# Optimization experiments

Hardware: AMD Instinct MI355X
Metric: run time of the kernel (lower is better)

The kernel has to match this reference:

```python
import jax, jax.numpy as jnp
import numpy as np

D_MODEL = 1024
NUM_HEADS = 16
HEAD_DIM = D_MODEL // NUM_HEADS
WINDOW = 256
NEG = -1000000000.0


def setup_inputs() -> dict:
    key = jax.random.key(0)
    ks = jax.random.split(key, 9)
    B, N, D = 2, 2048, D_MODEL
    s = 1.0 / np.sqrt(D)
    inp = {
        "x": jax.random.normal(ks[0], (B, N, D), dtype=jnp.float32),
        "Wq": jax.random.normal(ks[1], (D, D), dtype=jnp.float32) * s,
        "bq": jnp.zeros((D,), dtype=jnp.float32),
        "Wk": jax.random.normal(ks[2], (D, D), dtype=jnp.float32) * s,
        "bk": jnp.zeros((D,), dtype=jnp.float32),
        "Wv": jax.random.normal(ks[3], (D, D), dtype=jnp.float32) * s,
        "bv": jnp.zeros((D,), dtype=jnp.float32),
        "Wo": jax.random.normal(ks[4], (D, D), dtype=jnp.float32) * s,
        "bo": jnp.zeros((D,), dtype=jnp.float32),
    }
    return inp


def reference(x, Wq, bq, Wk, bk, Wv, bv, Wo, bo):
    B, N, D = x.shape
    H, hd = NUM_HEADS, HEAD_DIM
    q = (x @ Wq + bq).reshape(B, N, H, hd).transpose(0, 2, 1, 3)  # [B,H,N,hd]
    k = (x @ Wk + bk).reshape(B, N, H, hd).transpose(0, 2, 1, 3)
    v = (x @ Wv + bv).reshape(B, N, H, hd).transpose(0, 2, 1, 3)

    i = jnp.arange(N)[:, None]
    j = jnp.arange(N)[None, :]
    blocked = (j > i) | (j < i - WINDOW)  # causal + local window
    mask = jnp.where(blocked, jnp.float32(NEG), jnp.float32(0.0))  # [N,N]

    logits = jnp.einsum("bhid,bhjd->bhij", q, k) / jnp.sqrt(jnp.float32(hd))
    logits = logits + mask[None, None, :, :]
    attn = jax.nn.softmax(logits, axis=-1)
    out = jnp.einsum("bhij,bhjd->bhid", attn, v)  # [B,H,N,hd]
    out = out.transpose(0, 2, 1, 3).reshape(B, N, D)
    return out @ Wo + bo
```

## Files before the change

kernel.cpp:

```cpp
#include <hip/hip_runtime.h>


typedef unsigned short ushort_t;
typedef __bf16 bf16x8 __attribute__((ext_vector_type(8)));
typedef float f32x4 __attribute__((ext_vector_type(4)));
typedef unsigned short ushort8 __attribute__((ext_vector_type(8)));
typedef unsigned short ushort4v __attribute__((ext_vector_type(4)));

#define LOG2E 1.4426950408889634f

static __device__ __forceinline__ ushort_t f2b(float f) {
    union { float f; unsigned int u; } x;
    x.f = f;
    unsigned int u = x.u;
    unsigned int r = (u + 0x7FFFu + ((u >> 16) & 1u)) >> 16;
    return (ushort_t)r;
}

static __device__ __forceinline__ void store_out(float* p, float v) { *p = v; }
static __device__ __forceinline__ void store_out(ushort_t* p, float v) { *p = f2b(v); }

static __device__ __forceinline__ int sw(int row, int c) {
    return (row * 8 + (c ^ (row & 7))) * 8;
}

static __device__ __forceinline__ void gload_lds16(const ushort_t* g, ushort_t* l) {
    __builtin_amdgcn_global_load_lds(
        (const __attribute__((address_space(1))) void*)g,
        (__attribute__((address_space(3))) void*)l, 16, 0, 0);
}

__global__ __launch_bounds__(256) void prep_kernel(
    const float* __restrict__ x, ushort_t* __restrict__ xbf,
    const float* __restrict__ W0, const float* __restrict__ W1,
    const float* __restrict__ W2, const float* __restrict__ W3,
    ushort_t* __restrict__ T0, ushort_t* __restrict__ T1,
    ushort_t* __restrict__ T2, ushort_t* __restrict__ T3) {
    int tx = threadIdx.x, ty = threadIdx.y;
    if (blockIdx.z == 4) {
        int idx = (blockIdx.y * 32 + blockIdx.x) * 256 + ty * 32 + tx;
        int i = idx * 16;
#pragma unroll
        for (int half = 0; half < 2; half++) {
            f32x4 a = *(const f32x4*)&x[i + half * 8];
            f32x4 b = *(const f32x4*)&x[i + half * 8 + 4];
            ushort8 o;
#pragma unroll
            for (int e = 0; e < 4; e++) o[e] = f2b(a[e]);
#pragma unroll
            for (int e = 0; e < 4; e++) o[4 + e] = f2b(b[e]);
            *(ushort8*)&xbf[i + half * 8] = o;
        }
        return;
    }
    __shared__ ushort_t tile[32][33];
    const float* W;
    ushort_t* T;
    switch (blockIdx.z) {
        case 0: W = W0; T = T0; break;
        case 1: W = W1; T = T1; break;
        case 2: W = W2; T = T2; break;
        default: W = W3; T = T3; break;
    }
    int xx = blockIdx.x * 32 + tx;
    int ybase = blockIdx.y * 32 + ty;
#pragma unroll
    for (int r = 0; r < 4; r++) tile[ty + r * 8][tx] = f2b(W[(ybase + r * 8) * 1024 + xx]);
    __syncthreads();
    {
        int u = ty * 32 + tx;
        int ro = u >> 3;
        int cg = (u & 7) * 4;
        ushort4v o;
#pragma unroll
        for (int k = 0; k < 4; k++) o[k] = tile[cg + k][ro];
        *(ushort4v*)&T[(long)(blockIdx.x * 32 + ro) * 1024 + blockIdx.y * 32 + cg] = o;
    }
}

__global__ __launch_bounds__(256) void gemm_qkv_kernel(
    const ushort_t* __restrict__ A,
    const ushort_t* __restrict__ Bt0, const ushort_t* __restrict__ Bt1,
    const ushort_t* __restrict__ Bt2,
    const float* __restrict__ bias0, const float* __restrict__ bias1,
    const float* __restrict__ bias2,
    ushort_t* __restrict__ C0, ushort_t* __restrict__ C1, ushort_t* __restrict__ C2,
    float os0, float os1, float os2) {
    __shared__ ushort_t Al[64 * 64];
    __shared__ ushort_t Bl[128 * 64];

    const int id = blockIdx.x;
    const int xcd = id & 7;
    const int s = id >> 3;
    int m_blk = (xcd >> 1) * 16 + (s & 15);
    int ncol = (xcd & 1) * 12 + (s >> 4);
    int zsel = ncol >> 3;
    ncol &= 7;
    const int m0 = m_blk * 64;
    const int n0 = ncol * 128;

    const ushort_t* Bt;
    const float* bias;
    ushort_t* C;
    float oscale;
    if (zsel == 0) { Bt = Bt0; bias = bias0; C = C0; oscale = os0; }
    else if (zsel == 1) { Bt = Bt1; bias = bias1; C = C1; oscale = os1; }
    else { Bt = Bt2; bias = bias2; C = C2; oscale = os2; }

    const int tid = threadIdx.x;
    const int w = tid >> 6;
    const int l = tid & 63;
    const int wm = (w >> 1) * 32;
    const int wn = (w & 1) * 64;
    const int lrow = l & 15;
    const int lq = l >> 4;

    f32x4 acc[2][4];
#pragma unroll
    for (int mi = 0; mi < 2; mi++)
#pragma unroll
        for (int ni = 0; ni < 4; ni++) acc[mi][ni] = 0.0f;

    const int kt0 = (id * 5) & 15;
    for (int it = 0; it < 16; it++) {
        const int kt = ((kt0 + it) & 15) * 64;
#pragma unroll
        for (int t = 0; t < 2; t++) {
            int idx = t * 256 + tid;
            int row = idx >> 3, cs = idx & 7, c = cs ^ (row & 7);
            gload_lds16(&A[(long)(m0 + row) * 1024 + kt + c * 8], &Al[idx * 8]);
        }
#pragma unroll
        for (int t = 0; t < 4; t++) {
            int idx = t * 256 + tid;
            int row = idx >> 3, cs = idx & 7, c = cs ^ (row & 7);
            gload_lds16(&Bt[(long)(n0 + row) * 1024 + kt + c * 8], &Bl[idx * 8]);
        }
        __syncthreads();
#pragma unroll
        for (int ks = 0; ks < 64; ks += 32) {
            const int cb = (ks >> 3) + lq;
            bf16x8 af[2], bfr[4];
#pragma unroll
            for (int mi = 0; mi < 2; mi++)
                af[mi] = *(const bf16x8*)&Al[sw(wm + mi * 16 + lrow, cb)];
#pragma unroll
            for (int ni = 0; ni < 4; ni++)
                bfr[ni] = *(const bf16x8*)&Bl[sw(wn + ni * 16 + lrow, cb)];
#pragma unroll
            for (int mi = 0; mi < 2; mi++)
#pragma unroll
                for (int ni = 0; ni < 4; ni++)
                    acc[mi][ni] = __builtin_amdgcn_mfma_f32_16x16x32_bf16(
                        af[mi], bfr[ni], acc[mi][ni], 0, 0, 0);
        }
        __syncthreads();
    }

    if (zsel == 2) {
#pragma unroll
        for (int ni = 0; ni < 4; ni++) {
            int n = n0 + wn + ni * 16 + lrow;
            float bv = bias[n];
#pragma unroll
            for (int mi = 0; mi < 2; mi++) {
                int m = m0 + wm + mi * 16 + lq * 4;
                ushort4v o;
#pragma unroll
                for (int r = 0; r < 4; r++) o[r] = f2b((acc[mi][ni][r] + bv) * oscale);
                *(ushort4v*)&C[(long)n * 4096 + m] = o;
            }
        }
    } else {
#pragma unroll
        for (int ni = 0; ni < 4; ni++) {
            int n = n0 + wn + ni * 16 + lrow;
            float bv = bias[n];
#pragma unroll
            for (int mi = 0; mi < 2; mi++) {
#pragma unroll
                for (int r = 0; r < 4; r++) {
                    int m = m0 + wm + mi * 16 + lq * 4 + r;
                    store_out(&C[(long)m * 1024 + n], (acc[mi][ni][r] + bv) * oscale);
                }
            }
        }
    }
}

__global__ __launch_bounds__(256) void gemm_out_kernel(
    const ushort_t* __restrict__ A, const ushort_t* __restrict__ Bt,
    const float* __restrict__ bias, float* __restrict__ C) {
    __shared__ ushort_t Al[64 * 64];
    __shared__ ushort_t Bl[128 * 64];

    const int id = blockIdx.x;
    const int xcd = id & 7;
    const int s = id >> 3;
    const int m_blk = xcd * 8 + (s & 7);
    const int ncol = s >> 3;
    const int m0 = m_blk * 64;
    const int n0 = ncol * 128;

    const int tid = threadIdx.x;
    const int w = tid >> 6;
    const int l = tid & 63;
    const int wm = (w >> 1) * 32;
    const int wn = (w & 1) * 64;
    const int lrow = l & 15;
    const int lq = l >> 4;

    f32x4 acc[2][4];
#pragma unroll
    for (int mi = 0; mi < 2; mi++)
#pragma unroll
        for (int ni = 0; ni < 4; ni++) acc[mi][ni] = 0.0f;

    const int kt0 = (id * 5) & 15;
    for (int it = 0; it < 16; it++) {
        const int kt = ((kt0 + it) & 15) * 64;
#pragma unroll
        for (int t = 0; t < 2; t++) {
            int idx = t * 256 + tid;
            int row = idx >> 3, cs = idx & 7, c = cs ^ (row & 7);
            gload_lds16(&A[(long)(m0 + row) * 1024 + kt + c * 8], &Al[idx * 8]);
        }
#pragma unroll
        for (int t = 0; t < 4; t++) {
            int idx = t * 256 + tid;
            int row = idx >> 3, cs = idx & 7, c = cs ^ (row & 7);
            gload_lds16(&Bt[(long)(n0 + row) * 1024 + kt + c * 8], &Bl[idx * 8]);
        }
        __syncthreads();
#pragma unroll
        for (int ks = 0; ks < 64; ks += 32) {
            const int cb = (ks >> 3) + lq;
            bf16x8 af[2], bfr[4];
#pragma unroll
            for (int mi = 0; mi < 2; mi++)
                af[mi] = *(const bf16x8*)&Al[sw(wm + mi * 16 + lrow, cb)];
#pragma unroll
            for (int ni = 0; ni < 4; ni++)
                bfr[ni] = *(const bf16x8*)&Bl[sw(wn + ni * 16 + lrow, cb)];
#pragma unroll
            for (int mi = 0; mi < 2; mi++)
#pragma unroll
                for (int ni = 0; ni < 4; ni++)
                    acc[mi][ni] = __builtin_amdgcn_mfma_f32_16x16x32_bf16(
                        af[mi], bfr[ni], acc[mi][ni], 0, 0, 0);
        }
        __syncthreads();
    }

#pragma unroll
    for (int ni = 0; ni < 4; ni++) {
        int n = n0 + wn + ni * 16 + lrow;
        float bv = bias[n];
#pragma unroll
        for (int mi = 0; mi < 2; mi++) {
#pragma unroll
            for (int r = 0; r < 4; r++) {
                int m = m0 + wm + mi * 16 + lq * 4 + r;
                C[(long)m * 1024 + n] = acc[mi][ni][r] + bv;
            }
        }
    }
}

__global__ __launch_bounds__(256) void attn_kernel(
    const ushort_t* __restrict__ Q, const ushort_t* __restrict__ K,
    const ushort_t* __restrict__ VT, ushort_t* __restrict__ O) {
    __shared__ ushort_t Kl[128 * 64];
    __shared__ ushort_t Vtl[64 * 128];
    __shared__ ushort_t Pb[4 * 16 * 40];

    const int id = blockIdx.x;
    const int xcd = id & 7;
    const int s = id >> 3;
    const int bh = xcd * 4 + (s >> 5);
    const int b = bh >> 4;
    const int h = bh & 15;
    const int i0 = (s & 31) * 64;

    const int tid = threadIdx.x;
    const int w = tid >> 6;
    const int l = tid & 63;
    const int lrow = l & 15;
    const int lq = l >> 4;
    const int q0 = i0 + w * 16;

    const long baseBH = ((long)b * 2048) * 1024 + (long)h * 64;
    const long baseVT = (long)h * 64 * 4096 + (long)b * 2048;

    const ushort_t* qrow = Q + baseBH + (long)(q0 + lrow) * 1024;
    bf16x8 aq0 = *(const bf16x8*)&qrow[lq * 8];
    bf16x8 aq1 = *(const bf16x8*)&qrow[32 + lq * 8];

    float lpart[4];
    f32x4 oacc[4];
#pragma unroll
    for (int r = 0; r < 4; r++) lpart[r] = 0.0f;
#pragma unroll
    for (int ni = 0; ni < 4; ni++) oacc[ni] = 0.0f;

    const int kstart = (i0 - 256) > 0 ? (i0 - 256) : 0;
    const int kend = i0 + 64;
    ushort_t* Pw = &Pb[w * 16 * 40];

    for (int cs = kstart; cs < kend; cs += 128) {
        const int ce = (cs + 128 < kend) ? cs + 128 : kend;
#pragma unroll
        for (int t = 0; t < 4; t++) {
            int idx = t * 256 + tid;
            int rr = idx >> 3;
            int cc = idx & 7;
            int c = cc ^ (rr & 7);
            int key = cs + rr;
            key = key < 2047 ? key : 2047;
            gload_lds16(&K[baseBH + (long)key * 1024 + c * 8], &Kl[idx * 8]);
        }
#pragma unroll
        for (int t = 0; t < 4; t++) {
            int idx = t * 256 + tid;
            int rr = idx >> 4;
            int cc = idx & 15;
            int c = (cc & 8) | ((cc & 7) ^ (rr & 7));
            int kc = cs + c * 8;
            kc = kc < 2040 ? kc : 2040;
            gload_lds16(&VT[baseVT + (long)rr * 4096 + kc], &Vtl[idx * 8]);
        }
        __syncthreads();

        int pend = -1;
        for (int kb = cs; kb < ce; kb += 32) {
            if (kb > q0 + 15 || kb + 31 < q0 - 256) continue;
            const int rb = kb - cs;
            f32x4 S0 = 0.0f, S1 = 0.0f;
            {
                bf16x8 bk;
                bk = *(const bf16x8*)&Kl[sw(rb + lrow, lq)];
                S0 = __builtin_amdgcn_mfma_f32_16x16x32_bf16(aq0, bk, S0, 0, 0, 0);
                bk = *(const bf16x8*)&Kl[sw(rb + lrow, 4 + lq)];
                S0 = __builtin_amdgcn_mfma_f32_16x16x32_bf16(aq1, bk, S0, 0, 0, 0);
                bk = *(const bf16x8*)&Kl[sw(rb + 16 + lrow, lq)];
                S1 = __builtin_amdgcn_mfma_f32_16x16x32_bf16(aq0, bk, S1, 0, 0, 0);
                bk = *(const bf16x8*)&Kl[sw(rb + 16 + lrow, 4 + lq)];
                S1 = __builtin_amdgcn_mfma_f32_16x16x32_bf16(aq1, bk, S1, 0, 0, 0);
            }
            if (pend >= 0) {
                bf16x8 pf = *(const bf16x8*)&Pw[lrow * 40 + lq * 8];
#pragma unroll
                for (int ni = 0; ni < 4; ni++) {
                    int ccg = (pend >> 3) + lq;
                    int rsw = (ccg & 8) | ((ccg & 7) ^ (lrow & 7));
                    bf16x8 vf = *(const bf16x8*)&Vtl[(ni * 16 + lrow) * 128 + rsw * 8];
                    oacc[ni] = __builtin_amdgcn_mfma_f32_16x16x32_bf16(pf, vf, oacc[ni], 0, 0, 0);
                }
            }
            if (kb <= q0 - 31 && kb >= q0 - 241) {
#pragma unroll
                for (int r = 0; r < 4; r++) {
                    float p0 = exp2f(S0[r] * LOG2E);
                    float p1 = exp2f(S1[r] * LOG2E);
                    lpart[r] += p0 + p1;
                    const int prow = lq * 4 + r;
                    Pw[prow * 40 + lrow] = f2b(p0);
                    Pw[prow * 40 + 16 + lrow] = f2b(p1);
                }
            } else {
                const int col0 = kb + lrow;
                const int col1 = kb + 16 + lrow;
#pragma unroll
                for (int r = 0; r < 4; r++) {
                    const int i = q0 + lq * 4 + r;
                    float p0 = (col0 > i || col0 < i - 256) ? 0.0f : exp2f(S0[r] * LOG2E);
                    float p1 = (col1 > i || col1 < i - 256) ? 0.0f : exp2f(S1[r] * LOG2E);
                    lpart[r] += p0 + p1;
                    const int prow = lq * 4 + r;
                    Pw[prow * 40 + lrow] = f2b(p0);
                    Pw[prow * 40 + 16 + lrow] = f2b(p1);
                }
            }
            pend = rb;
        }
        if (pend >= 0) {
            bf16x8 pf = *(const bf16x8*)&Pw[lrow * 40 + lq * 8];
#pragma unroll
            for (int ni = 0; ni < 4; ni++) {
                int ccg = (pend >> 3) + lq;
                int rsw = (ccg & 8) | ((ccg & 7) ^ (lrow & 7));
                bf16x8 vf = *(const bf16x8*)&Vtl[(ni * 16 + lrow) * 128 + rsw * 8];
                oacc[ni] = __builtin_amdgcn_mfma_f32_16x16x32_bf16(pf, vf, oacc[ni], 0, 0, 0);
            }
        }
        __syncthreads();
    }

    float lS[4];
#pragma unroll
    for (int r = 0; r < 4; r++) {
        float rs = lpart[r];
#pragma unroll
        for (int off = 8; off; off >>= 1) rs += __shfl_xor(rs, off, 64);
        lS[r] = rs;
    }

#pragma unroll
    for (int ni = 0; ni < 4; ni++) {
#pragma unroll
        for (int r = 0; r < 4; r++) {
            const int i = q0 + lq * 4 + r;
            const int d = ni * 16 + lrow;
            O[baseBH + (long)i * 1024 + d] = f2b(oacc[ni][r] / lS[r]);
        }
    }
}

extern "C" void kernel_launch(void* const* d_in, const int* in_sizes, int n_in,
                              void* d_out, int out_size, void* d_ws, size_t ws_size,
                              hipStream_t stream) {
    const float* x  = (const float*)d_in[0];
    const float* Wq = (const float*)d_in[1];
    const float* bq = (const float*)d_in[2];
    const float* Wk = (const float*)d_in[3];
    const float* bk = (const float*)d_in[4];
    const float* Wv = (const float*)d_in[5];
    const float* bv = (const float*)d_in[6];
    const float* Wo = (const float*)d_in[7];
    const float* bo = (const float*)d_in[8];
    float* out = (float*)d_out;

    ushort_t* ws = (ushort_t*)d_ws;
    const size_t WMAT = (size_t)1024 * 1024;
    const size_t ACT = (size_t)2 * 2048 * 1024;
    ushort_t* xbf = ws;
    ushort_t* Wqt = xbf + ACT;
    ushort_t* Wkt = Wqt + WMAT;
    ushort_t* Wvt = Wkt + WMAT;
    ushort_t* Wot = Wvt + WMAT;
    ushort_t* qws = Wot + WMAT;
    ushort_t* kws = qws + ACT;
    ushort_t* vws = kws + ACT;
    ushort_t* aws = xbf;

    prep_kernel<<<dim3(32, 32, 5), dim3(32, 8), 0, stream>>>(
        x, xbf, Wq, Wk, Wv, Wo, Wqt, Wkt, Wvt, Wot);

    gemm_qkv_kernel<<<1536, 256, 0, stream>>>(
        xbf, Wqt, Wkt, Wvt, bq, bk, bv, qws, kws, vws, 0.125f, 1.0f, 1.0f);

    attn_kernel<<<1024, 256, 0, stream>>>(qws, kws, vws, aws);

    gemm_out_kernel<<<512, 256, 0, stream>>>(aws, Wot, bo, out);
}
```

Baseline: 162.4 us.

## Process 128 queries per attention block, two 16-row tiles per wave

The attention kernel now gives each block 128 query rows and each wave 32 rows, split into two 16-row MFMA tiles that share the K and V fragments read from LDS. The grid is halved and each K/V chunk staged in shared memory is reused by twice as many queries, which cuts global loads and LDS traffic per output row. Since every chunk now lies fully in range, the index clamps are dropped. The cost is more registers per wave (two sets of accumulators and Q fragments) and fewer blocks to spread across the GPU, which could lower occupancy.

```diff
diff --git a/kernel.cpp b/kernel.cpp
--- a/kernel.cpp
+++ b/kernel.cpp
@@ -272,52 +272,53 @@
     const ushort_t* __restrict__ VT, ushort_t* __restrict__ O) {
     __shared__ ushort_t Kl[128 * 64];
     __shared__ ushort_t Vtl[64 * 128];
-    __shared__ ushort_t Pb[4 * 16 * 40];
+    __shared__ ushort_t Pb[4 * 2 * 640];
 
     const int id = blockIdx.x;
     const int xcd = id & 7;
     const int s = id >> 3;
-    const int bh = xcd * 4 + (s >> 5);
+    const int bh = xcd * 4 + (s >> 4);
     const int b = bh >> 4;
     const int h = bh & 15;
-    const int i0 = (s & 31) * 64;
+    const int i0 = (s & 15) * 128;
 
     const int tid = threadIdx.x;
     const int w = tid >> 6;
     const int l = tid & 63;
     const int lrow = l & 15;
     const int lq = l >> 4;
-    const int q0 = i0 + w * 16;
+    const int q0 = i0 + w * 32;
 
     const long baseBH = ((long)b * 2048) * 1024 + (long)h * 64;
     const long baseVT = (long)h * 64 * 4096 + (long)b * 2048;
 
-    const ushort_t* qrow = Q + baseBH + (long)(q0 + lrow) * 1024;
-    bf16x8 aq0 = *(const bf16x8*)&qrow[lq * 8];
-    bf16x8 aq1 = *(const bf16x8*)&qrow[32 + lq * 8];
-
-    float lpart[4];
-    f32x4 oacc[4];
-#pragma unroll
-    for (int r = 0; r < 4; r++) lpart[r] = 0.0f;
-#pragma unroll
-    for (int ni = 0; ni < 4; ni++) oacc[ni] = 0.0f;
+    const ushort_t* qrowA = Q + baseBH + (long)(q0 + lrow) * 1024;
+    const ushort_t* qrowB = qrowA + 16 * 1024;
+    bf16x8 aq0 = *(const bf16x8*)&qrowA[lq * 8];
+    bf16x8 aq1 = *(const bf16x8*)&qrowA[32 + lq * 8];
+    bf16x8 aq2 = *(const bf16x8*)&qrowB[lq * 8];
+    bf16x8 aq3 = *(const bf16x8*)&qrowB[32 + lq * 8];
+
+    float lpartA[4], lpartB[4];
+    f32x4 oaccA[4], oaccB[4];
+#pragma unroll
+    for (int r = 0; r < 4; r++) { lpartA[r] = 0.0f; lpartB[r] = 0.0f; }
+#pragma unroll
+    for (int ni = 0; ni < 4; ni++) { oaccA[ni] = 0.0f; oaccB[ni] = 0.0f; }
 
     const int kstart = (i0 - 256) > 0 ? (i0 - 256) : 0;
-    const int kend = i0 + 64;
-    ushort_t* Pw = &Pb[w * 16 * 40];
+    const int kend = i0 + 128;
+    ushort_t* Pw0 = &Pb[w * 2 * 640];
+    ushort_t* Pw1 = Pw0 + 640;
 
     for (int cs = kstart; cs < kend; cs += 128) {
-        const int ce = (cs + 128 < kend) ? cs + 128 : kend;
 #pragma unroll
         for (int t = 0; t < 4; t++) {
             int idx = t * 256 + tid;
             int rr = idx >> 3;
             int cc = idx & 7;
             int c = cc ^ (rr & 7);
-            int key = cs + rr;
-            key = key < 2047 ? key : 2047;
-            gload_lds16(&K[baseBH + (long)key * 1024 + c * 8], &Kl[idx * 8]);
+            gload_lds16(&K[baseBH + (long)(cs + rr) * 1024 + c * 8], &Kl[idx * 8]);
         }
 #pragma unroll
         for (int t = 0; t < 4; t++) {
@@ -325,93 +326,116 @@
             int rr = idx >> 4;
             int cc = idx & 15;
             int c = (cc & 8) | ((cc & 7) ^ (rr & 7));
-            int kc = cs + c * 8;
-            kc = kc < 2040 ? kc : 2040;
-            gload_lds16(&VT[baseVT + (long)rr * 4096 + kc], &Vtl[idx * 8]);
+            gload_lds16(&VT[baseVT + (long)rr * 4096 + cs + c * 8], &Vtl[idx * 8]);
         }
         __syncthreads();
 
         int pend = -1;
+        const int ce = cs + 128;
         for (int kb = cs; kb < ce; kb += 32) {
-            if (kb > q0 + 15 || kb + 31 < q0 - 256) continue;
+            if (kb > q0 + 31 || kb + 31 < q0 - 256) continue;
             const int rb = kb - cs;
-            f32x4 S0 = 0.0f, S1 = 0.0f;
+            f32x4 S0a = 0.0f, S1a = 0.0f, S0b = 0.0f, S1b = 0.0f;
             {
-                bf16x8 bk;
-                bk = *(const bf16x8*)&Kl[sw(rb + lrow, lq)];
-                S0 = __builtin_amdgcn_mfma_f32_16x16x32_bf16(aq0, bk, S0, 0, 0, 0);
-                bk = *(const bf16x8*)&Kl[sw(rb + lrow, 4 + lq)];
-                S0 = __builtin_amdgcn_mfma_f32_16x16x32_bf16(aq1, bk, S0, 0, 0, 0);
-                bk = *(const bf16x8*)&Kl[sw(rb + 16 + lrow, lq)];
-                S1 = __builtin_amdgcn_mfma_f32_16x16x32_bf16(aq0, bk, S1, 0, 0, 0);
-                bk = *(const bf16x8*)&Kl[sw(rb + 16 + lrow, 4 + lq)];
-                S1 = __builtin_amdgcn_mfma_f32_16x16x32_bf16(aq1, bk, S1, 0, 0, 0);
+                bf16x8 bk0 = *(const bf16x8*)&Kl[sw(rb + lrow, lq)];
+                bf16x8 bk1 = *(const bf16x8*)&Kl[sw(rb + lrow, 4 + lq)];
+                bf16x8 bk2 = *(const bf16x8*)&Kl[sw(rb + 16 + lrow, lq)];
+                bf16x8 bk3 = *(const bf16x8*)&Kl[sw(rb + 16 + lrow, 4 + lq)];
+                S0a = __builtin_amdgcn_mfma_f32_16x16x32_bf16(aq0, bk0, S0a, 0, 0, 0);
+                S0a = __builtin_amdgcn_mfma_f32_16x16x32_bf16(aq1, bk1, S0a, 0, 0, 0);
+                S1a = __builtin_amdgcn_mfma_f32_16x16x32_bf16(aq0, bk2, S1a, 0, 0, 0);
+                S1a = __builtin_amdgcn_mfma_f32_16x16x32_bf16(aq1, bk3, S1a, 0, 0, 0);
+                S0b = __builtin_amdgcn_mfma_f32_16x16x32_bf16(aq2, bk0, S0b, 0, 0, 0);
+                S0b = __builtin_amdgcn_mfma_f32_16x16x32_bf16(aq3, bk1, S0b, 0, 0, 0);
+                S1b = __builtin_amdgcn_mfma_f32_16x16x32_bf16(aq2, bk2, S1b, 0, 0, 0);
+                S1b = __builtin_amdgcn_mfma_f32_16x16x32_bf16(aq3, bk3, S1b, 0, 0, 0);
             }
             if (pend >= 0) {
-                bf16x8 pf = *(const bf16x8*)&Pw[lrow * 40 + lq * 8];
+                bf16x8 pf0 = *(const bf16x8*)&Pw0[lrow * 40 + lq * 8];
+                bf16x8 pf1 = *(const bf16x8*)&Pw1[lrow * 40 + lq * 8];
 #pragma unroll
                 for (int ni = 0; ni < 4; ni++) {
                     int ccg = (pend >> 3) + lq;
                     int rsw = (ccg & 8) | ((ccg & 7) ^ (lrow & 7));
                     bf16x8 vf = *(const bf16x8*)&Vtl[(ni * 16 + lrow) * 128 + rsw * 8];
-                    oacc[ni] = __builtin_amdgcn_mfma_f32_16x16x32_bf16(pf, vf, oacc[ni], 0, 0, 0);
+                    oaccA[ni] = __builtin_amdgcn_mfma_f32_16x16x32_bf16(pf0, vf, oaccA[ni], 0, 0, 0);
+                    oaccB[ni] = __builtin_amdgcn_mfma_f32_16x16x32_bf16(pf1, vf, oaccB[ni], 0, 0, 0);
                 }
             }
-            if (kb <= q0 - 31 && kb >= q0 - 241) {
+            if (kb <= q0 - 31 && kb >= q0 - 225) {
 #pragma unroll
                 for (int r = 0; r < 4; r++) {
-                    float p0 = exp2f(S0[r] * LOG2E);
-                    float p1 = exp2f(S1[r] * LOG2E);
-                    lpart[r] += p0 + p1;
+                    float p0a = exp2f(S0a[r] * LOG2E);
+                    float p1a = exp2f(S1a[r] * LOG2E);
+                    float p0b = exp2f(S0b[r] * LOG2E);
+                    float p1b = exp2f(S1b[r] * LOG2E);
+                    lpartA[r] += p0a + p1a;
+                    lpartB[r] += p0b + p1b;
                     const int prow = lq * 4 + r;
-                    Pw[prow * 40 + lrow] = f2b(p0);
-                    Pw[prow * 40 + 16 + lrow] = f2b(p1);
+                    Pw0[prow * 40 + lrow] = f2b(p0a);
+                    Pw0[prow * 40 + 16 + lrow] = f2b(p1a);
+                    Pw1[prow * 40 + lrow] = f2b(p0b);
+                    Pw1[prow * 40 + 16 + lrow] = f2b(p1b);
                 }
             } else {
                 const int col0 = kb + lrow;
                 const int col1 = kb + 16 + lrow;
 #pragma unroll
                 for (int r = 0; r < 4; r++) {
-                    const int i = q0 + lq * 4 + r;
-                    float p0 = (col0 > i || col0 < i - 256) ? 0.0f : exp2f(S0[r] * LOG2E);
-                    float p1 = (col1 > i || col1 < i - 256) ? 0.0f : exp2f(S1[r] * LOG2E);
-                    lpart[r] += p0 + p1;
+                    const int ia = q0 + lq * 4 + r;
+                    const int ib = ia + 16;
+                    float p0a = (col0 > ia || col0 < ia - 256) ? 0.0f : exp2f(S0a[r] * LOG2E);
+                    float p1a = (col1 > ia || col1 < ia - 256) ? 0.0f : exp2f(S1a[r] * LOG2E);
+                    float p0b = (col0 > ib || col0 < ib - 256) ? 0.0f : exp2f(S0b[r] * LOG2E);
+                    float p1b = (col1 > ib || col1 < ib - 256) ? 0.0f : exp2f(S1b[r] * LOG2E);
+                    lpartA[r] += p0a + p1a;
+                    lpartB[r] += p0b + p1b;
                     const int prow = lq * 4 + r;
-                    Pw[prow * 40 + lrow] = f2b(p0);
-                    Pw[prow * 40 + 16 + lrow] = f2b(p1);
+                    Pw0[prow * 40 + lrow] = f2b(p0a);
+                    Pw0[prow * 40 + 16 + lrow] = f2b(p1a);
+                    Pw1[prow * 40 + lrow] = f2b(p0b);
+                    Pw1[prow * 40 + 16 + lrow] = f2b(p1b);
                 }
             }
             pend = rb;
         }
         if (pend >= 0) {
-            bf16x8 pf = *(const bf16x8*)&Pw[lrow * 40 + lq * 8];
+            bf16x8 pf0 = *(const bf16x8*)&Pw0[lrow * 40 + lq * 8];
+            bf16x8 pf1 = *(const bf16x8*)&Pw1[lrow * 40 + lq * 8];
 #pragma unroll
             for (int ni = 0; ni < 4; ni++) {
                 int ccg = (pend >> 3) + lq;
                 int rsw = (ccg & 8) | ((ccg & 7) ^ (lrow & 7));
                 bf16x8 vf = *(const bf16x8*)&Vtl[(ni * 16 + lrow) * 128 + rsw * 8];
-                oacc[ni] = __builtin_amdgcn_mfma_f32_16x16x32_bf16(pf, vf, oacc[ni], 0, 0, 0);
-            }
-        }
-        __syncthreads();
-    }
-
-    float lS[4];
+                oaccA[ni] = __builtin_amdgcn_mfma_f32_16x16x32_bf16(pf0, vf, oaccA[ni], 0, 0, 0);
+                oaccB[ni] = __builtin_amdgcn_mfma_f32_16x16x32_bf16(pf1, vf, oaccB[ni], 0, 0, 0);
+            }
+        }
+        __syncthreads();
+    }
+
+    float lSA[4], lSB[4];
 #pragma unroll
     for (int r = 0; r < 4; r++) {
-        float rs = lpart[r];
-#pragma unroll
-        for (int off = 8; off; off >>= 1) rs += __shfl_xor(rs, off, 64);
-        lS[r] = rs;
+        float ra = lpartA[r];
+        float rb2 = lpartB[r];
+#pragma unroll
+        for (int off = 8; off; off >>= 1) {
+            ra += __shfl_xor(ra, off, 64);
+            rb2 += __shfl_xor(rb2, off, 64);
+        }
+        lSA[r] = ra;
+        lSB[r] = rb2;
     }
 
 #pragma unroll
     for (int ni = 0; ni < 4; ni++) {
 #pragma unroll
         for (int r = 0; r < 4; r++) {
-            const int i = q0 + lq * 4 + r;
+            const int ia = q0 + lq * 4 + r;
             const int d = ni * 16 + lrow;
-            O[baseBH + (long)i * 1024 + d] = f2b(oacc[ni][r] / lS[r]);
+            O[baseBH + (long)ia * 1024 + d] = f2b(oaccA[ni][r] / lSA[r]);
+            O[baseBH + (long)(ia + 16) * 1024 + d] = f2b(oaccB[ni][r] / lSB[r]);
         }
     }
 }
@@ -449,7 +473,7 @@
     gemm_qkv_kernel<<<1536, 256, 0, stream>>>(
         xbf, Wqt, Wkt, Wvt, bq, bk, bv, qws, kws, vws, 0.125f, 1.0f, 1.0f);
 
-    attn_kernel<<<1024, 256, 0, stream>>>(qws, kws, vws, aws);
+    attn_kernel<<<512, 256, 0, stream>>>(qws, kws, vws, aws);
 
     gemm_out_kernel<<<512, 256, 0, stream>>>(aws, Wot, bo, out);
 }
```

After: 161.9 us. About the same (-0.3%).
